# Optimization experiments

Measured on AMD Instinct MI355X. Metric: run time of the kernel, lower is better.

The kernel has to match this reference:

```python
import jax, jax.numpy as jnp
import numpy as np

B = 16; H = 64; WRES = 64; C = 512; NH = 16; WH = 8; WW = 8; PATCH = 4
N = WH * WW; HD = C // NH; R_MAX = PATCH * H; HID = 4 * C
PI = 3.141592653589793


def _rel_coords():
    yy, xx = np.meshgrid(np.arange(WH), np.arange(WW), indexing='ij')
    flat = np.stack([yy.ravel(), xx.ravel()])  # (2, N)
    rel = flat[:, :, None] - flat[:, None, :]  # (2, N, N)
    return rel[0].astype(np.int32), rel[1].astype(np.int32)

RAD_NP, AZ_NP = _rel_coords()


def _ln(x, g, b):
    m = x.mean(-1, keepdims=True)
    v = ((x - m) ** 2).mean(-1, keepdims=True)
    return (x - m) / jnp.sqrt(v + 1e-5) * g + b


def setup_inputs() -> dict:
    key = jax.random.key(0)
    ks = jax.random.split(key, 12)
    s = 0.02
    return {
        'x': jax.random.normal(ks[0], (B, H * WRES, C), jnp.float32),
        'D': jax.random.uniform(ks[1], (B, H, WRES), jnp.float32),
        'norm1_g': jnp.ones((C,), jnp.float32), 'norm1_b': jnp.zeros((C,), jnp.float32),
        'qkv_w': jax.random.normal(ks[2], (3 * C, C), jnp.float32) * s,
        'qkv_b': jnp.zeros((3 * C,), jnp.float32),
        'proj_w': jax.random.normal(ks[3], (C, C), jnp.float32) * s,
        'proj_b': jnp.zeros((C,), jnp.float32),
        'a_p': jax.random.normal(ks[4], (2 * WW - 1, NH), jnp.float32) * s,
        'b_p': jax.random.normal(ks[5], (2 * WW - 1, NH), jnp.float32) * s,
        'a_r': jax.random.normal(ks[6], (2 * WH - 1, NH), jnp.float32) * s,
        'b_r': jax.random.normal(ks[7], (2 * WH - 1, NH), jnp.float32) * s,
        'norm2_g': jnp.ones((C,), jnp.float32), 'norm2_b': jnp.zeros((C,), jnp.float32),
        'fc1_w': jax.random.normal(ks[8], (HID, C), jnp.float32) * s,
        'fc1_b': jnp.zeros((HID,), jnp.float32),
        'fc2_w': jax.random.normal(ks[9], (C, HID), jnp.float32) * s,
        'fc2_b': jnp.zeros((C,), jnp.float32),
    }


def reference(x, D, norm1_g, norm1_b, qkv_w, qkv_b, proj_w, proj_b,
              a_p, b_p, a_r, b_r, norm2_g, norm2_b, fc1_w, fc1_b, fc2_w, fc2_b):
    rad = jnp.asarray(RAD_NP)  # (N, N) relative row offsets in [-(WH-1), WH-1]
    az = jnp.asarray(AZ_NP)    # (N, N) relative col offsets
    shortcut = x
    xn = _ln(x, norm1_g, norm1_b).reshape(B, H, WRES, C)
    # window partition: (B,H,W,C) -> (nW*B, N, C); same for D -> (nW*B, N)
    xw = xn.reshape(B, H // WH, WH, WRES // WW, WW, C).transpose(0, 1, 3, 2, 4, 5).reshape(-1, N, C)
    Dw = D.reshape(B, H // WH, WH, WRES // WW, WW).transpose(0, 1, 3, 2, 4).reshape(-1, N)
    # qkv: (B_, N, 3C) -> q,k,v (B_, NH, N, HD)
    qkv = (xw @ qkv_w.T + qkv_b).reshape(-1, N, 3, NH, HD).transpose(2, 0, 3, 1, 4)
    q, k, v = qkv[0], qkv[1], qkv[2]
    q = q * (HD ** -0.5)
    attn = jnp.einsum('bhnd,bhmd->bhnm', q, k)
    # A_phi: gathered azimuth tables + trig, (N, N, NH). torch negative index == idx % size
    ip = az % (2 * WW - 1)
    azf = az.astype(jnp.float32) * (2.0 * PI / WRES)
    A_phi = a_p[ip] * jnp.cos(azf)[..., None] + b_p[ip] * jnp.sin(azf)[..., None]
    # A_r: per-window depth-modulated radius, (B_, N, N, NH); rad_final[b,i,j] = rad[i,j]*D[b,j]
    ir = rad % (2 * WH - 1)
    ang = (rad.astype(jnp.float32)[None] * Dw[:, None, :]) * (2.0 * PI / R_MAX)
    A_r = a_r[ir][None] * jnp.cos(ang)[..., None] + b_r[ir][None] * jnp.sin(ang)[..., None]
    attn = attn + jnp.transpose(A_phi, (2, 0, 1))[None] + jnp.transpose(A_r, (0, 3, 1, 2))
    attn = jax.nn.softmax(attn, axis=-1)
    out = jnp.einsum('bhnm,bhmd->bhnd', attn, v).transpose(0, 2, 1, 3).reshape(-1, N, C)
    out = out @ proj_w.T + proj_b
    # window reverse -> (B, H*W, C)
    xr = out.reshape(B, H // WH, WRES // WW, WH, WW, C).transpose(0, 1, 3, 2, 4, 5).reshape(B, H * WRES, C)
    x = shortcut + xr
    xm = _ln(x, norm2_g, norm2_b)
    h = jax.nn.gelu(xm @ fc1_w.T + fc1_b, approximate=False)
    return x + (h @ fc2_w.T + fc2_b)
```

## Files before the change

### kernel.cpp

```cpp
#include <hip/hip_runtime.h>
#include <hip/hip_bf16.h>
#include <math.h>

typedef __hip_bfloat16 bf16;
using f32x4  = __attribute__((ext_vector_type(4))) float;
using bf16x8 = __attribute__((ext_vector_type(8))) short;

static __device__ __forceinline__ float b2f(bf16 v) { return __bfloat162float(v); }
static __device__ __forceinline__ short f2b_s(float f) {
    bf16 b = __float2bfloat16(f);
    return *reinterpret_cast<short*>(&b);
}

static __device__ __forceinline__ void gl_lds16(const void* g, void* l) {
    __builtin_amdgcn_global_load_lds(
        (const __attribute__((address_space(1))) unsigned int*)g,
        (__attribute__((address_space(3))) unsigned int*)l, 16, 0, 0);
}

__global__ __launch_bounds__(256) void f2b_kernel(const float* __restrict__ in,
                                                  short* __restrict__ out, int n4)
{
    int i = blockIdx.x * 256 + threadIdx.x;
    if (i < n4) {
        float4 f = reinterpret_cast<const float4*>(in)[i];
        short4 s;
        s.x = f2b_s(f.x); s.y = f2b_s(f.y); s.z = f2b_s(f.z); s.w = f2b_s(f.w);
        reinterpret_cast<short4*>(out)[i] = s;
    }
}

__global__ __launch_bounds__(64) void ln_kernel(
    const float* __restrict__ in, const float* __restrict__ g,
    const float* __restrict__ bta, bf16* __restrict__ out, int windowed)
{
    int lr  = blockIdx.x;
    int tid = threadIdx.x;
    const float* xr = in + (size_t)lr * 512;
    int c0 = tid * 8;
    float4 f0 = *reinterpret_cast<const float4*>(xr + c0);
    float4 f1 = *reinterpret_cast<const float4*>(xr + c0 + 4);
    float v[8] = { f0.x, f0.y, f0.z, f0.w, f1.x, f1.y, f1.z, f1.w };
    float s = 0.f, s2 = 0.f;
#pragma unroll
    for (int k = 0; k < 8; ++k) { s += v[k]; s2 += v[k] * v[k]; }
#pragma unroll
    for (int off = 32; off; off >>= 1) {
        s  += __shfl_xor(s,  off, 64);
        s2 += __shfl_xor(s2, off, 64);
    }
    float mean = s * (1.0f / 512.0f);
    float var  = s2 * (1.0f / 512.0f) - mean * mean;
    float inv  = rsqrtf(var + 1e-5f);
    size_t drow;
    if (windowed) {
        int b_loc = lr >> 12;
        int l  = lr & 4095;
        int gr = l >> 6, gc = l & 63;
        int wy = gr >> 3, iy = gr & 7, wx = gc >> 3, ix = gc & 7;
        drow = (size_t)((b_loc * 64 + wy * 8 + wx) * 64 + iy * 8 + ix);
    } else {
        drow = (size_t)lr;
    }
    bf16* orow = out + drow * 512;
#pragma unroll
    for (int k = 0; k < 8; ++k) {
        int c = c0 + k;
        orow[c] = __float2bfloat16((v[k] - mean) * inv * g[c] + bta[c]);
    }
}

__global__ __launch_bounds__(256) void gemm_mfma(
    const bf16* __restrict__ A, const short* __restrict__ W,
    const float* __restrict__ bias, int N, int K, int mode,
    void* __restrict__ dstv, const float* __restrict__ res)
{
    __shared__ short Asl[128 * 32];
    __shared__ short Bsl[128 * 32];

    int tid  = threadIdx.x;
    int wave = tid >> 6, lane = tid & 63;
    int waveM = wave >> 1, waveN = wave & 1;
    int mBase = blockIdx.y * 128;
    int nBase = blockIdx.x * 128;

    f32x4 acc[4][4] = {};

    int rr   = wave * 32 + (lane >> 2);
    int segE = (lane & 3) * 8;
    const bf16*  Ag = A + (size_t)(mBase + rr) * K + segE;
    const short* Bg = W + (size_t)(nBase + rr) * K + segE;
    short* Al0 = &Asl[wave * 1024];
    short* Bl0 = &Bsl[wave * 1024];

    int mf = waveM * 64 + (lane & 15);
    int nf = waveN * 64 + (lane & 15);
    int kq = (lane >> 4) * 8;

    for (int kb = 0; kb < K; kb += 32) {
        gl_lds16(Ag + kb,               Al0);
        gl_lds16(Ag + kb + (size_t)16 * K, Al0 + 512);
        gl_lds16(Bg + kb,               Bl0);
        gl_lds16(Bg + kb + (size_t)16 * K, Bl0 + 512);
        __syncthreads();

        bf16x8 af[4], bfv[4];
#pragma unroll
        for (int i = 0; i < 4; ++i)
            af[i] = *reinterpret_cast<const bf16x8*>(&Asl[(mf + i * 16) * 32 + kq]);
#pragma unroll
        for (int j = 0; j < 4; ++j)
            bfv[j] = *reinterpret_cast<const bf16x8*>(&Bsl[(nf + j * 16) * 32 + kq]);
#pragma unroll
        for (int i = 0; i < 4; ++i)
#pragma unroll
            for (int j = 0; j < 4; ++j)
                acc[i][j] = __builtin_amdgcn_mfma_f32_16x16x32_bf16(af[i], bfv[j], acc[i][j], 0, 0, 0);
        __syncthreads();
    }

    int rq = (lane >> 4) * 4;
#pragma unroll
    for (int j = 0; j < 4; ++j) {
        int n = nBase + waveN * 64 + j * 16 + (lane & 15);
        float bn = bias[n];
#pragma unroll
        for (int i = 0; i < 4; ++i) {
#pragma unroll
            for (int reg = 0; reg < 4; ++reg) {
                int m = mBase + waveM * 64 + i * 16 + rq + reg;
                float v = acc[i][j][reg] + bn;
                if (mode == 0) {
                    ((bf16*)dstv)[(size_t)m * N + n] = __float2bfloat16(v);
                } else if (mode == 1) {
                    int b_loc = m >> 12, w = (m >> 6) & 63, tk = m & 63;
                    int wy = w >> 3, wx = w & 7, iy = tk >> 3, ix = tk & 7;
                    int l = ((wy << 3) + iy) * 64 + (wx << 3) + ix;
                    size_t idx = ((size_t)(b_loc * 4096 + l)) * 512 + n;
                    ((float*)dstv)[idx] = v + res[idx];
                } else if (mode == 2) {
                    float gl = 0.5f * v * (1.0f + erff(v * 0.70710678118654752f));
                    ((bf16*)dstv)[(size_t)m * N + n] = __float2bfloat16(gl);
                } else {
                    size_t idx = (size_t)m * N + n;
                    ((float*)dstv)[idx] = v + res[idx];
                }
            }
        }
    }
}

__global__ __launch_bounds__(256) void attn_kernel(
    const bf16* __restrict__ qkv, const float* __restrict__ Dofs,
    const float* __restrict__ a_p, const float* __restrict__ b_p,
    const float* __restrict__ a_r, const float* __restrict__ b_r,
    bf16* __restrict__ xattn)
{
    __shared__ float cosr[15][64];
    __shared__ float sinr[15][64];
    __shared__ float aphiS[15][16];
    __shared__ float arsS[15][16];
    __shared__ float brsS[15][16];
    __shared__ short Vt[32][72];
    __shared__ short Psh[64][72];

    int b_ = blockIdx.x;
    int bl = b_ >> 6;
    int w  = b_ & 63;
    int wy = w >> 3, wx = w & 7;
    int tid  = threadIdx.x;
    int wave = tid >> 6, lane = tid & 63;

    const float scale = 0.17677669529663687f;
    const float c_az  = 0.09817477042468103f;
    const float c_r   = 0.02454369260617026f;

    for (int t = tid; t < 960; t += 256) {
        int k = t >> 6;
        int j = t & 63;
        int jy = j >> 3, jx = j & 7;
        float Dj  = Dofs[(size_t)bl * 4096 + (wy * 8 + jy) * 64 + (wx * 8 + jx)];
        float ang = (float)(k - 7) * Dj * c_r;
        cosr[k][j] = __cosf(ang);
        sinr[k][j] = __sinf(ang);
    }
    if (tid < 240) {
        int k = tid >> 4;
        int h = tid & 15;
        int v = k - 7;
        int ip = v < 0 ? v + 15 : v;
        float azf = (float)v * c_az;
        aphiS[k][h] = a_p[ip * 16 + h] * __cosf(azf) + b_p[ip * 16 + h] * __sinf(azf);
        arsS[k][h]  = a_r[ip * 16 + h];
        brsS[k][h]  = b_r[ip * 16 + h];
    }

    int i_blk = wave;
    int l15 = lane & 15;
    int lq  = lane >> 4;
    int m0  = i_blk * 16 + lq * 4;
    const bf16* qbase = qkv + (size_t)(b_ * 64) * 1536;
    bf16* obase = xattn + (size_t)(b_ * 64) * 512;

    for (int h = 0; h < 16; ++h) {
        __syncthreads();
        {
            int tok = tid >> 2, dc = (tid & 3) * 8;
            bf16x8 vv = *reinterpret_cast<const bf16x8*>(
                qkv + (size_t)(b_ * 64 + tok) * 1536 + 1024 + h * 32 + dc);
#pragma unroll
            for (int s = 0; s < 8; ++s) Vt[dc + s][tok] = vv[s];
        }
        __syncthreads();

        bf16x8 af = *reinterpret_cast<const bf16x8*>(
            qbase + (size_t)(i_blk * 16 + l15) * 1536 + h * 32 + lq * 8);
        f32x4 Sacc[4] = {};
#pragma unroll
        for (int jb = 0; jb < 4; ++jb) {
            bf16x8 kf = *reinterpret_cast<const bf16x8*>(
                qbase + (size_t)(jb * 16 + l15) * 1536 + 512 + h * 32 + lq * 8);
            Sacc[jb] = __builtin_amdgcn_mfma_f32_16x16x32_bf16(af, kf, Sacc[jb], 0, 0, 0);
        }

        float Sv[4][4];
        float inv[4];
#pragma unroll
        for (int reg = 0; reg < 4; ++reg) {
            int m = m0 + reg;
            int iy = m >> 3, ix = m & 7;
            float rmax = -1e30f;
#pragma unroll
            for (int jb = 0; jb < 4; ++jb) {
                int n = jb * 16 + l15;
                int jy = n >> 3, jx = n & 7;
                int ai = ix - jx + 7;
                int ri = iy - jy + 7;
                float sc = Sacc[jb][reg] * scale + aphiS[ai][h]
                         + arsS[ri][h] * cosr[ri][n] + brsS[ri][h] * sinr[ri][n];
                Sv[reg][jb] = sc;
                rmax = fmaxf(rmax, sc);
            }
#pragma unroll
            for (int off = 1; off <= 8; off <<= 1)
                rmax = fmaxf(rmax, __shfl_xor(rmax, off, 64));
            float rsum = 0.f;
#pragma unroll
            for (int jb = 0; jb < 4; ++jb) {
                float e = __expf(Sv[reg][jb] - rmax);
                Sv[reg][jb] = e;
                rsum += e;
            }
#pragma unroll
            for (int off = 1; off <= 8; off <<= 1)
                rsum += __shfl_xor(rsum, off, 64);
            inv[reg] = 1.0f / rsum;
        }

#pragma unroll
        for (int reg = 0; reg < 4; ++reg)
#pragma unroll
            for (int jb = 0; jb < 4; ++jb)
                Psh[m0 + reg][jb * 16 + l15] = f2b_s(Sv[reg][jb]);

        f32x4 o[2] = {};
#pragma unroll
        for (int ks = 0; ks < 2; ++ks) {
            bf16x8 pa = *reinterpret_cast<const bf16x8*>(
                &Psh[i_blk * 16 + l15][ks * 32 + lq * 8]);
#pragma unroll
            for (int nb = 0; nb < 2; ++nb) {
                bf16x8 bv = *reinterpret_cast<const bf16x8*>(
                    &Vt[nb * 16 + l15][ks * 32 + lq * 8]);
                o[nb] = __builtin_amdgcn_mfma_f32_16x16x32_bf16(pa, bv, o[nb], 0, 0, 0);
            }
        }

#pragma unroll
        for (int nb = 0; nb < 2; ++nb) {
            int d = nb * 16 + l15;
#pragma unroll
            for (int reg = 0; reg < 4; ++reg) {
                int m = m0 + reg;
                obase[(size_t)m * 512 + h * 32 + d] = __float2bfloat16(o[nb][reg] * inv[reg]);
            }
        }
    }
}

extern "C" void kernel_launch(void* const* d_in, const int* in_sizes, int n_in,
                              void* d_out, int out_size, void* d_ws, size_t ws_size,
                              hipStream_t stream)
{
    const float* x      = (const float*)d_in[0];
    const float* D      = (const float*)d_in[1];
    const float* n1g    = (const float*)d_in[2];
    const float* n1b    = (const float*)d_in[3];
    const float* qkv_w  = (const float*)d_in[4];
    const float* qkv_b  = (const float*)d_in[5];
    const float* proj_w = (const float*)d_in[6];
    const float* proj_b = (const float*)d_in[7];
    const float* a_p    = (const float*)d_in[8];
    const float* b_p    = (const float*)d_in[9];
    const float* a_r    = (const float*)d_in[10];
    const float* b_r    = (const float*)d_in[11];
    const float* n2g    = (const float*)d_in[12];
    const float* n2b    = (const float*)d_in[13];
    const float* fc1_w  = (const float*)d_in[14];
    const float* fc1_b  = (const float*)d_in[15];
    const float* fc2_w  = (const float*)d_in[16];
    const float* fc2_b  = (const float*)d_in[17];
    float* out = (float*)d_out;

    char* ws = (char*)d_ws;
    short* qkv_wb  = (short*)ws;
    short* proj_wb = qkv_wb + 786432;
    short* fc1_wb  = proj_wb + 262144;
    short* fc2_wb  = fc1_wb + 1048576;
    char* gws = (char*)(fc2_wb + 1048576);

    int G = 16;
    while (G > 1 && 6291456 + (size_t)G * 4096 * 7168 > ws_size) G >>= 1;
    int NG = 16 / G;
    size_t rowsA = (size_t)G * 4096;

    float* x2   = (float*)gws;
    bf16*  xw   = (bf16*)(gws + rowsA * 2048);
    bf16*  qkvb = xw + rowsA * 512;
    bf16*  xatt = qkvb + rowsA * 1536;
    bf16*  xm   = xw;
    bf16*  hbuf = qkvb;

    hipLaunchKernelGGL(f2b_kernel, dim3(768),  dim3(256), 0, stream, qkv_w,  qkv_wb,  196608);
    hipLaunchKernelGGL(f2b_kernel, dim3(256),  dim3(256), 0, stream, proj_w, proj_wb,  65536);
    hipLaunchKernelGGL(f2b_kernel, dim3(1024), dim3(256), 0, stream, fc1_w,  fc1_wb,  262144);
    hipLaunchKernelGGL(f2b_kernel, dim3(1024), dim3(256), 0, stream, fc2_w,  fc2_wb,  262144);

    int gy = (int)(rowsA / 128);

    for (int g = 0; g < NG; ++g) {
        size_t r0 = (size_t)g * rowsA;
        hipLaunchKernelGGL(ln_kernel, dim3((int)rowsA), dim3(64), 0, stream,
                           x + r0 * 512, n1g, n1b, xw, 1);
        hipLaunchKernelGGL(gemm_mfma, dim3(1536 / 128, gy), dim3(256), 0, stream,
                           xw, qkv_wb, qkv_b, 1536, 512, 0, (void*)qkvb, (const float*)nullptr);
        hipLaunchKernelGGL(attn_kernel, dim3(G * 64), dim3(256), 0, stream,
                           qkvb, D + r0, a_p, b_p, a_r, b_r, xatt);
        hipLaunchKernelGGL(gemm_mfma, dim3(512 / 128, gy), dim3(256), 0, stream,
                           xatt, proj_wb, proj_b, 512, 512, 1, (void*)x2, x + r0 * 512);
        hipLaunchKernelGGL(ln_kernel, dim3((int)rowsA), dim3(64), 0, stream,
                           x2, n2g, n2b, xm, 0);
        hipLaunchKernelGGL(gemm_mfma, dim3(2048 / 128, gy), dim3(256), 0, stream,
                           xm, fc1_wb, fc1_b, 2048, 512, 2, (void*)hbuf, (const float*)nullptr);
        hipLaunchKernelGGL(gemm_mfma, dim3(512 / 128, gy), dim3(256), 0, stream,
                           hbuf, fc2_wb, fc2_b, 512, 2048, 3, (void*)(out + r0 * 512), x2);
    }
}
```

Baseline: 1.417 ms.

## Double-buffer GEMM LDS tiles, remap workgroups, and raise MFMA wave priority

Splits the GEMM's LDS tiles into two buffers so the next K-slice is loaded with global_load_lds while MFMAs run on the current slice, leaving one barrier per iteration instead of two. Workgroup IDs are also remapped in strides of eight, likely to group blocks for cache locality or across XCDs. s_setprio is raised around the MFMA block. This doubles LDS use per block, which may lower occupancy, and the single barrier relies on the async LDS writes finishing before the next read.

```diff
diff --git a/kernel.cpp b/kernel.cpp
--- a/kernel.cpp
+++ b/kernel.cpp
@@ -75,14 +75,20 @@
     const float* __restrict__ bias, int N, int K, int mode,
     void* __restrict__ dstv, const float* __restrict__ res)
 {
-    __shared__ short Asl[128 * 32];
-    __shared__ short Bsl[128 * 32];
+    __shared__ short Asl[2][128 * 32];
+    __shared__ short Bsl[2][128 * 32];
 
     int tid  = threadIdx.x;
     int wave = tid >> 6, lane = tid & 63;
     int waveM = wave >> 1, waveN = wave & 1;
-    int mBase = blockIdx.y * 128;
-    int nBase = blockIdx.x * 128;
+
+    int nx  = gridDim.x;
+    int nwg = nx * gridDim.y;
+    int lid = blockIdx.y * nx + blockIdx.x;
+    int nid = lid;
+    if ((nwg & 7) == 0) nid = (lid & 7) * (nwg >> 3) + (lid >> 3);
+    int mBase = (nid / nx) * 128;
+    int nBase = (nid % nx) * 128;
 
     f32x4 acc[4][4] = {};
 
@@ -90,33 +96,60 @@
     int segE = (lane & 3) * 8;
     const bf16*  Ag = A + (size_t)(mBase + rr) * K + segE;
     const short* Bg = W + (size_t)(nBase + rr) * K + segE;
-    short* Al0 = &Asl[wave * 1024];
-    short* Bl0 = &Bsl[wave * 1024];
+
+    short* curA = &Asl[0][wave * 1024];
+    short* curB = &Bsl[0][wave * 1024];
+    short* nxtA = &Asl[1][wave * 1024];
+    short* nxtB = &Bsl[1][wave * 1024];
 
     int mf = waveM * 64 + (lane & 15);
     int nf = waveN * 64 + (lane & 15);
     int kq = (lane >> 4) * 8;
+    int mro = (mf - wave * 1024 / 32);
+
+    short* curAf = &Asl[0][0];
+    short* curBf = &Bsl[0][0];
+    short* nxtAf = &Asl[1][0];
+    short* nxtBf = &Bsl[1][0];
+
+    gl_lds16(Ag,               curA);
+    gl_lds16(Ag + (size_t)16 * K, curA + 512);
+    gl_lds16(Bg,               curB);
+    gl_lds16(Bg + (size_t)16 * K, curB + 512);
+    __syncthreads();
 
     for (int kb = 0; kb < K; kb += 32) {
-        gl_lds16(Ag + kb,               Al0);
-        gl_lds16(Ag + kb + (size_t)16 * K, Al0 + 512);
-        gl_lds16(Bg + kb,               Bl0);
-        gl_lds16(Bg + kb + (size_t)16 * K, Bl0 + 512);
-        __syncthreads();
+        bool more = (kb + 32 < K);
+        if (more) {
+            gl_lds16(Ag + kb + 32,                 nxtA);
+            gl_lds16(Ag + kb + 32 + (size_t)16 * K, nxtA + 512);
+            gl_lds16(Bg + kb + 32,                 nxtB);
+            gl_lds16(Bg + kb + 32 + (size_t)16 * K, nxtB + 512);
+        }
 
         bf16x8 af[4], bfv[4];
 #pragma unroll
         for (int i = 0; i < 4; ++i)
-            af[i] = *reinterpret_cast<const bf16x8*>(&Asl[(mf + i * 16) * 32 + kq]);
+            af[i] = *reinterpret_cast<const bf16x8*>(&curAf[(mf + i * 16) * 32 + kq]);
 #pragma unroll
         for (int j = 0; j < 4; ++j)
-            bfv[j] = *reinterpret_cast<const bf16x8*>(&Bsl[(nf + j * 16) * 32 + kq]);
+            bfv[j] = *reinterpret_cast<const bf16x8*>(&curBf[(nf + j * 16) * 32 + kq]);
+
+        __builtin_amdgcn_s_setprio(1);
 #pragma unroll
         for (int i = 0; i < 4; ++i)
 #pragma unroll
             for (int j = 0; j < 4; ++j)
                 acc[i][j] = __builtin_amdgcn_mfma_f32_16x16x32_bf16(af[i], bfv[j], acc[i][j], 0, 0, 0);
-        __syncthreads();
+        __builtin_amdgcn_s_setprio(0);
+
+        if (more) __syncthreads();
+
+        short* t;
+        t = curA; curA = nxtA; nxtA = t;
+        t = curB; curB = nxtB; nxtB = t;
+        t = curAf; curAf = nxtAf; nxtAf = t;
+        t = curBf; curBf = nxtBf; nxtBf = t;
     }
 
     int rq = (lane >> 4) * 4;
```

After: 1.595 ms. 1.13x slower.

## Load GEMM fragments directly from global memory and remap workgroups for XCD locality

Applied to the files above, without the earlier changes.

The GEMM no longer stages A and B tiles through LDS with global_load_lds and two barriers per k-step. Each wave now reads its MFMA fragments straight from global memory, relying on L1/L2 to serve the reuse between the two waves that share each tile. Workgroup IDs are also permuted so that consecutive tiles land on the same XCD, which is meant to improve L2 sharing. The trade is more global/L1 traffic and less latency hiding, since there is no explicit staging or prefetch, in exchange for removing the barriers and LDS traffic.

```diff
diff --git a/kernel.cpp b/kernel.cpp
--- a/kernel.cpp
+++ b/kernel.cpp
@@ -10,12 +10,6 @@
 static __device__ __forceinline__ short f2b_s(float f) {
     bf16 b = __float2bfloat16(f);
     return *reinterpret_cast<short*>(&b);
-}
-
-static __device__ __forceinline__ void gl_lds16(const void* g, void* l) {
-    __builtin_amdgcn_global_load_lds(
-        (const __attribute__((address_space(1))) unsigned int*)g,
-        (__attribute__((address_space(3))) unsigned int*)l, 16, 0, 0);
 }
 
 __global__ __launch_bounds__(256) void f2b_kernel(const float* __restrict__ in,
@@ -75,54 +69,47 @@
     const float* __restrict__ bias, int N, int K, int mode,
     void* __restrict__ dstv, const float* __restrict__ res)
 {
-    __shared__ short Asl[128 * 32];
-    __shared__ short Bsl[128 * 32];
-
     int tid  = threadIdx.x;
     int wave = tid >> 6, lane = tid & 63;
     int waveM = wave >> 1, waveN = wave & 1;
-    int mBase = blockIdx.y * 128;
-    int nBase = blockIdx.x * 128;
+
+    int nx  = gridDim.x;
+    int nwg = nx * gridDim.y;
+    int lid = blockIdx.y * nx + blockIdx.x;
+    int nid = lid;
+    if ((nwg & 7) == 0) nid = (lid & 7) * (nwg >> 3) + (lid >> 3);
+    int mBase = (nid / nx) * 128;
+    int nBase = (nid % nx) * 128;
+
+    int l15 = lane & 15;
+    int kq  = (lane >> 4) * 8;
+
+    const bf16*  A0 = A + (size_t)(mBase + waveM * 64 + l15) * K + kq;
+    const short* B0 = W + (size_t)(nBase + waveN * 64 + l15) * K + kq;
+    size_t rs = (size_t)16 * K;
 
     f32x4 acc[4][4] = {};
 
-    int rr   = wave * 32 + (lane >> 2);
-    int segE = (lane & 3) * 8;
-    const bf16*  Ag = A + (size_t)(mBase + rr) * K + segE;
-    const short* Bg = W + (size_t)(nBase + rr) * K + segE;
-    short* Al0 = &Asl[wave * 1024];
-    short* Bl0 = &Bsl[wave * 1024];
-
-    int mf = waveM * 64 + (lane & 15);
-    int nf = waveN * 64 + (lane & 15);
-    int kq = (lane >> 4) * 8;
-
+#pragma unroll 2
     for (int kb = 0; kb < K; kb += 32) {
-        gl_lds16(Ag + kb,               Al0);
-        gl_lds16(Ag + kb + (size_t)16 * K, Al0 + 512);
-        gl_lds16(Bg + kb,               Bl0);
-        gl_lds16(Bg + kb + (size_t)16 * K, Bl0 + 512);
-        __syncthreads();
-
         bf16x8 af[4], bfv[4];
 #pragma unroll
         for (int i = 0; i < 4; ++i)
-            af[i] = *reinterpret_cast<const bf16x8*>(&Asl[(mf + i * 16) * 32 + kq]);
+            af[i] = *reinterpret_cast<const bf16x8*>(A0 + rs * i + kb);
 #pragma unroll
         for (int j = 0; j < 4; ++j)
-            bfv[j] = *reinterpret_cast<const bf16x8*>(&Bsl[(nf + j * 16) * 32 + kq]);
+            bfv[j] = *reinterpret_cast<const bf16x8*>(B0 + rs * j + kb);
 #pragma unroll
         for (int i = 0; i < 4; ++i)
 #pragma unroll
             for (int j = 0; j < 4; ++j)
                 acc[i][j] = __builtin_amdgcn_mfma_f32_16x16x32_bf16(af[i], bfv[j], acc[i][j], 0, 0, 0);
-        __syncthreads();
     }
 
     int rq = (lane >> 4) * 4;
 #pragma unroll
     for (int j = 0; j < 4; ++j) {
-        int n = nBase + waveN * 64 + j * 16 + (lane & 15);
+        int n = nBase + waveN * 64 + j * 16 + l15;
         float bn = bias[n];
 #pragma unroll
         for (int i = 0; i < 4; ++i) {
```

After: 2.026 ms. 1.43x slower.

## Double-buffer GEMM LDS tiles and remap workgroups across XCDs

Applied to the files above, without the earlier changes.

The bf16 MFMA GEMM now uses two LDS buffers, so the global-to-LDS loads for the next K step are issued before the MFMAs on the current step run. This hides load latency and removes one barrier per step. Workgroup IDs are also remapped in groups of 8, so neighbouring tiles land on the same XCD, which should improve L2 reuse. The cost is doubled LDS use, which may lower occupancy, and the loop assumes the number of K steps is even.

```diff
diff --git a/kernel.cpp b/kernel.cpp
--- a/kernel.cpp
+++ b/kernel.cpp
@@ -75,14 +75,22 @@
     const float* __restrict__ bias, int N, int K, int mode,
     void* __restrict__ dstv, const float* __restrict__ res)
 {
-    __shared__ short Asl[128 * 32];
-    __shared__ short Bsl[128 * 32];
+    __shared__ short As0[128 * 32];
+    __shared__ short Bs0[128 * 32];
+    __shared__ short As1[128 * 32];
+    __shared__ short Bs1[128 * 32];
 
     int tid  = threadIdx.x;
     int wave = tid >> 6, lane = tid & 63;
     int waveM = wave >> 1, waveN = wave & 1;
-    int mBase = blockIdx.y * 128;
-    int nBase = blockIdx.x * 128;
+
+    int nx  = gridDim.x;
+    int nwg = nx * gridDim.y;
+    int lid = blockIdx.y * nx + blockIdx.x;
+    int nid = lid;
+    if ((nwg & 7) == 0) nid = (lid & 7) * (nwg >> 3) + (lid >> 3);
+    int mBase = (nid / nx) * 128;
+    int nBase = (nid % nx) * 128;
 
     f32x4 acc[4][4] = {};
 
@@ -90,33 +98,47 @@
     int segE = (lane & 3) * 8;
     const bf16*  Ag = A + (size_t)(mBase + rr) * K + segE;
     const short* Bg = W + (size_t)(nBase + rr) * K + segE;
-    short* Al0 = &Asl[wave * 1024];
-    short* Bl0 = &Bsl[wave * 1024];
+    size_t rs16 = (size_t)16 * K;
 
     int mf = waveM * 64 + (lane & 15);
     int nf = waveN * 64 + (lane & 15);
     int kq = (lane >> 4) * 8;
 
-    for (int kb = 0; kb < K; kb += 32) {
-        gl_lds16(Ag + kb,               Al0);
-        gl_lds16(Ag + kb + (size_t)16 * K, Al0 + 512);
-        gl_lds16(Bg + kb,               Bl0);
-        gl_lds16(Bg + kb + (size_t)16 * K, Bl0 + 512);
-        __syncthreads();
-
+    auto stage = [&](int kb, short* Ad, short* Bd) {
+        gl_lds16(Ag + kb,        Ad + wave * 1024);
+        gl_lds16(Ag + kb + rs16, Ad + wave * 1024 + 512);
+        gl_lds16(Bg + kb,        Bd + wave * 1024);
+        gl_lds16(Bg + kb + rs16, Bd + wave * 1024 + 512);
+    };
+    auto compute = [&](const short* As_, const short* Bs_) {
         bf16x8 af[4], bfv[4];
 #pragma unroll
         for (int i = 0; i < 4; ++i)
-            af[i] = *reinterpret_cast<const bf16x8*>(&Asl[(mf + i * 16) * 32 + kq]);
+            af[i] = *reinterpret_cast<const bf16x8*>(&As_[(mf + i * 16) * 32 + kq]);
 #pragma unroll
         for (int j = 0; j < 4; ++j)
-            bfv[j] = *reinterpret_cast<const bf16x8*>(&Bsl[(nf + j * 16) * 32 + kq]);
+            bfv[j] = *reinterpret_cast<const bf16x8*>(&Bs_[(nf + j * 16) * 32 + kq]);
 #pragma unroll
         for (int i = 0; i < 4; ++i)
 #pragma unroll
             for (int j = 0; j < 4; ++j)
                 acc[i][j] = __builtin_amdgcn_mfma_f32_16x16x32_bf16(af[i], bfv[j], acc[i][j], 0, 0, 0);
-        __syncthreads();
+    };
+
+    stage(0, As0, Bs0);
+    asm volatile("s_waitcnt vmcnt(0)" ::: "memory");
+    __builtin_amdgcn_s_barrier();
+
+    int nsteps = K >> 5;
+    for (int t = 0; t < nsteps; t += 2) {
+        stage((t + 1) << 5, As1, Bs1);
+        compute(As0, Bs0);
+        asm volatile("s_waitcnt vmcnt(0)" ::: "memory");
+        __builtin_amdgcn_s_barrier();
+        if (t + 2 < nsteps) stage((t + 2) << 5, As0, Bs0);
+        compute(As1, Bs1);
+        asm volatile("s_waitcnt vmcnt(0)" ::: "memory");
+        __builtin_amdgcn_s_barrier();
     }
 
     int rq = (lane >> 4) * 4;
```

Measured after the change: 1.418 ms. About the same (+0.1%).
